# Optimization experiments

Measured on AMD Instinct MI355X. Metric: run time of the kernel, lower is better.

Reference implementation:

```python
import jax, jax.numpy as jnp
import numpy as np

N_NODES = 100000
N_EDGES = 1600000
N_GRAPHS = 1024
F_IN, H = 128, 32  # num_node_features, hidden_channels


def setup_inputs() -> dict:
    key = jax.random.key(0)
    ks = jax.random.split(key, 12)
    x = jax.random.normal(ks[0], (N_NODES, F_IN), dtype=jnp.float32)
    edge_index = jax.random.randint(ks[1], (2, N_EDGES), 0, N_NODES, dtype=jnp.int64)
    batch = jnp.sort(jax.random.randint(ks[2], (N_NODES,), 0, N_GRAPHS, dtype=jnp.int64))
    def lin(k, fi, fo):
        s = 1.0 / np.sqrt(fi)
        return jax.random.uniform(k, (fi, fo), jnp.float32, -s, s)
    return {
        "x": x, "edge_index": edge_index, "batch": batch,
        "W1": lin(ks[3], F_IN, H),      "b1": jnp.zeros((H,), jnp.float32),
        "W2": lin(ks[4], H, 2 * H),     "b2": jnp.zeros((2 * H,), jnp.float32),
        "W3": lin(ks[5], 2 * H, 4 * H), "b3": jnp.zeros((4 * H,), jnp.float32),
        "W_lin": lin(ks[6], 4 * H, 1),  "b_lin": jnp.zeros((1,), jnp.float32),
    }


def _gcn_conv(x, W, b, src, dst, dinv):
    # PyG GCNConv: x' = x @ W; add self-loops; sym-normalized scatter-add; + bias
    h = x @ W                                   # [N, Fo]
    coef = (dinv[src] * dinv[dst])[:, None]      # [E, 1]
    out = jax.ops.segment_sum(h[src] * coef, dst, num_segments=x.shape[0])
    out = out + h * (dinv * dinv)[:, None]       # self-loop contribution
    return out + b


def reference(x, edge_index, batch, W1, b1, W2, b2, W3, b3, W_lin, b_lin):
    src, dst = edge_index[0], edge_index[1]
    n = x.shape[0]
    # degree with self-loops (edge_weight = 1)
    deg = jax.ops.segment_sum(jnp.ones((src.shape[0],), x.dtype), dst, num_segments=n) + 1.0
    dinv = jax.lax.rsqrt(deg)
    h = jax.nn.relu(_gcn_conv(x, W1, b1, src, dst, dinv))
    h = jax.nn.relu(_gcn_conv(h, W2, b2, src, dst, dinv))
    h = _gcn_conv(h, W3, b3, src, dst, dinv)
    # global_mean_pool over graph ids
    sums = jax.ops.segment_sum(h, batch, num_segments=N_GRAPHS)
    cnts = jax.ops.segment_sum(jnp.ones((n,), h.dtype), batch, num_segments=N_GRAPHS)
    pooled = sums / jnp.maximum(cnts, 1.0)[:, None]
    # dropout skipped (inference / training=False)
    return pooled @ W_lin + b_lin
```

## Files before the change

### kernel.cpp

```cpp
#include <hip/hip_runtime.h>

static constexpr int F_IN = 128;
static constexpr int H1 = 32;
static constexpr int TPB = 256;
static constexpr int MAXBKT = 2048;

__global__ void bcount_kernel(const int* __restrict__ dst, int* __restrict__ bcnt,
                              int E, int nbkt) {
    __shared__ int h[MAXBKT];
    for (int t = threadIdx.x; t < nbkt; t += TPB) h[t] = 0;
    __syncthreads();
    const int CH = (E + gridDim.x - 1) / gridDim.x;
    const int lo = blockIdx.x * CH;
    const int hi = min(lo + CH, E);
    for (int i = lo + threadIdx.x; i < hi; i += TPB) atomicAdd(&h[dst[i] >> 6], 1);
    __syncthreads();
    for (int tt = threadIdx.x; tt < nbkt; tt += TPB) {
        int t = tt + blockIdx.x * 613;
        t -= (t >= nbkt) ? nbkt * (t / nbkt) : 0;
        if (h[t]) atomicAdd(&bcnt[t], h[t]);
    }
}

__global__ void bscan_kernel(const int* __restrict__ bcnt, int* __restrict__ bptr,
                             int* __restrict__ bcur, int nbkt, int E) {
    __shared__ int sh[512];
    __shared__ int carry;
    if (threadIdx.x == 0) carry = 0;
    __syncthreads();
    for (int base = 0; base < nbkt; base += 512) {
        int t = base + threadIdx.x;
        int v = (t < nbkt) ? bcnt[t] : 0;
        sh[threadIdx.x] = v;
        __syncthreads();
        for (int o = 1; o < 512; o <<= 1) {
            int u = (threadIdx.x >= o) ? sh[threadIdx.x - o] : 0;
            __syncthreads();
            sh[threadIdx.x] += u;
            __syncthreads();
        }
        if (t < nbkt) {
            int excl = carry + sh[threadIdx.x] - v;
            bptr[t] = excl;
            bcur[t] = excl;
        }
        __syncthreads();
        if (threadIdx.x == 0) carry += sh[511];
        __syncthreads();
    }
    if (threadIdx.x == 0) bptr[nbkt] = E;
}

__global__ void bfill_kernel(const int* __restrict__ src, const int* __restrict__ dst,
                             int* __restrict__ bcur, int* __restrict__ packed,
                             int E, int nbkt) {
    __shared__ int h[MAXBKT];
    for (int t = threadIdx.x; t < nbkt; t += TPB) h[t] = 0;
    __syncthreads();
    const int CH = (E + gridDim.x - 1) / gridDim.x;
    const int lo = blockIdx.x * CH;
    const int hi = min(lo + CH, E);
    for (int i = lo + threadIdx.x; i < hi; i += TPB) atomicAdd(&h[dst[i] >> 6], 1);
    __syncthreads();
    for (int tt = threadIdx.x; tt < nbkt; tt += TPB) {
        int t = tt + blockIdx.x * 613;
        t -= (t >= nbkt) ? nbkt * (t / nbkt) : 0;
        int c = h[t];
        h[t] = c ? atomicAdd(&bcur[t], c) : 0;
    }
    __syncthreads();
    for (int i = lo + threadIdx.x; i < hi; i += TPB) {
        int d = dst[i];
        int slot = atomicAdd(&h[d >> 6], 1);
        packed[slot] = (src[i] << 6) | (d & 63);
    }
}

__global__ void localize_kernel(const int* __restrict__ bptr, const int* __restrict__ packed,
                                int* __restrict__ csr_src, int* __restrict__ degi,
                                int* __restrict__ rowptr, float* __restrict__ dinv, int N) {
    __shared__ int lcnt[64];
    __shared__ int lcur[64];
    const int b = blockIdx.x;
    const int lo = bptr[b], hi = bptr[b + 1];
    if (threadIdx.x < 64) lcnt[threadIdx.x] = 0;
    __syncthreads();
    for (int i = lo + threadIdx.x; i < hi; i += TPB) atomicAdd(&lcnt[packed[i] & 63], 1);
    __syncthreads();
    if (threadIdx.x < 64) {
        int v = lcnt[threadIdx.x];
        int s = v;
#pragma unroll
        for (int o = 1; o < 64; o <<= 1) {
            int u = __shfl_up(s, o, 64);
            if ((threadIdx.x & 63) >= (unsigned)o) s += u;
        }
        int excl = s - v;
        lcur[threadIdx.x] = lo + excl;
        int node = b * 64 + threadIdx.x;
        if (node < N) {
            rowptr[node] = lo + excl;
            degi[node] = v;
            dinv[node] = 1.0f / sqrtf((float)v + 1.0f);
        }
    }
    __syncthreads();
    for (int i = lo + threadIdx.x; i < hi; i += TPB) {
        int e = packed[i];
        int slot = atomicAdd(&lcur[e & 63], 1);
        csr_src[slot] = e >> 6;
    }
}

__global__ void prep_kernel(const float* __restrict__ W3, const float* __restrict__ b3,
                            const float* __restrict__ Wl, const float* __restrict__ bl,
                            float* __restrict__ w3l) {
    int j = threadIdx.x;
    float acc = 0.0f;
#pragma unroll
    for (int k = 0; k < 128; ++k) acc = fmaf(W3[j * 128 + k], Wl[k], acc);
    w3l[j] = acc;
    if (j == 0) {
        float beta = bl[0];
        for (int f = 0; f < 128; ++f) beta = fmaf(b3[f], Wl[f], beta);
        w3l[64] = beta;
    }
}

__global__ void gemm1_kernel(const float* __restrict__ X, const float* __restrict__ W,
                             const float* __restrict__ dinv, float* __restrict__ T, int N) {
    __shared__ float S[4224];
    float* Ws = S;
    float (*Os)[36] = reinterpret_cast<float(*)[36]>(S);
    for (int t = threadIdx.x; t < F_IN * H1; t += TPB) Ws[t] = W[t];
    __syncthreads();
    const int c16 = threadIdx.x & 15;
    const int kh  = (threadIdx.x >> 4) & 1;
    const int g   = threadIdx.x >> 5;
    const int base = blockIdx.x * 64;
    const int r0 = base + g * 8;
    const int k4o = kh * 16;
    const float4* xr[8];
#pragma unroll
    for (int i = 0; i < 8; ++i) {
        int row = r0 + i;
        if (row >= N) row = N - 1;
        xr[i] = reinterpret_cast<const float4*>(X + (size_t)row * F_IN);
    }
    float acc0[8] = {0, 0, 0, 0, 0, 0, 0, 0};
    float acc1[8] = {0, 0, 0, 0, 0, 0, 0, 0};
#pragma unroll 4
    for (int k4 = 0; k4 < 16; ++k4) {
        const int kk = (k4 + k4o) * 4;
        float wa0 = Ws[(kk + 0) * H1 + c16];
        float wa1 = Ws[(kk + 1) * H1 + c16];
        float wa2 = Ws[(kk + 2) * H1 + c16];
        float wa3 = Ws[(kk + 3) * H1 + c16];
        float wb0 = Ws[(kk + 0) * H1 + c16 + 16];
        float wb1 = Ws[(kk + 1) * H1 + c16 + 16];
        float wb2 = Ws[(kk + 2) * H1 + c16 + 16];
        float wb3 = Ws[(kk + 3) * H1 + c16 + 16];
#pragma unroll
        for (int i = 0; i < 8; ++i) {
            float4 xv = xr[i][k4 + k4o];
            acc0[i] = fmaf(xv.x, wa0, acc0[i]);
            acc0[i] = fmaf(xv.y, wa1, acc0[i]);
            acc0[i] = fmaf(xv.z, wa2, acc0[i]);
            acc0[i] = fmaf(xv.w, wa3, acc0[i]);
            acc1[i] = fmaf(xv.x, wb0, acc1[i]);
            acc1[i] = fmaf(xv.y, wb1, acc1[i]);
            acc1[i] = fmaf(xv.z, wb2, acc1[i]);
            acc1[i] = fmaf(xv.w, wb3, acc1[i]);
        }
    }
#pragma unroll
    for (int i = 0; i < 8; ++i) {
        acc0[i] += __shfl_xor(acc0[i], 16);
        acc1[i] += __shfl_xor(acc1[i], 16);
    }
    __syncthreads();
    const int myc = c16 + kh * 16;
#pragma unroll
    for (int i = 0; i < 8; ++i) {
        int row = r0 + i;
        float dv = dinv[row < N ? row : (N - 1)];
        float v = kh ? acc1[i] : acc0[i];
        Os[g * 8 + i][myc] = v * dv;
    }
    __syncthreads();
#pragma unroll
    for (int it = 0; it < 2; ++it) {
        int flat = it * 256 + threadIdx.x;
        int f4 = (flat & 1) * 4;
        int row = (flat >> 1) & 63;
        int s = flat >> 7;
        int grow = base + row;
        if (grow < N) {
            float4 v = *reinterpret_cast<const float4*>(&Os[row][s * 8 + f4]);
            *reinterpret_cast<float4*>(&T[((size_t)s * N + grow) * 8 + f4]) = v;
        }
    }
}

template <bool HASBIAS>
__global__ void gather_s(const int* __restrict__ rowptr, const int* __restrict__ degi,
                         const int* __restrict__ csr, const float* __restrict__ dinv,
                         const float* __restrict__ b, const float* __restrict__ Tin,
                         float* __restrict__ Tout, int N) {
    const int cls = blockIdx.x & 3;
    const int b4 = blockIdx.x >> 2;
    const int nb4 = gridDim.x >> 2;
    const int f = threadIdx.x & 7;
    const int cl = threadIdx.x >> 3;
    const float* __restrict__ tab = Tin + (size_t)cls * N * 8;
    float* __restrict__ outp = Tout + (size_t)cls * N * 8;
    const float bias = HASBIAS ? b[cls * 8 + f] : 0.0f;
    for (int node = b4 * 32 + cl; node < N; node += nb4 * 32) {
        float dv = dinv[node];
        float acc = tab[(size_t)node * 8 + f];
        int j = rowptr[node];
        const int end = j + degi[node];
        for (; j + 8 <= end; j += 8) {
            int sidx = csr[j + f];
#pragma unroll
            for (int k = 0; k < 8; ++k) {
                int s = __shfl(sidx, k, 8);
                acc += tab[(size_t)s * 8 + f];
            }
        }
        if (j < end) {
            int myIdx = j + f;
            int sidx = (myIdx < end) ? csr[myIdx] : -1;
#pragma unroll
            for (int k = 0; k < 8; ++k) {
                int s = __shfl(sidx, k, 8);
                if (s >= 0) acc += tab[(size_t)s * 8 + f];
            }
        }
        float v;
        if (HASBIAS) v = fmaxf(fmaf(acc, dv, bias), 0.0f) * dv;
        else         v = acc * dv;
        outp[(size_t)node * 8 + f] = v;
    }
}

__global__ void gemm2z_kernel(const float* __restrict__ S1s, const float* __restrict__ W2,
                              const float* __restrict__ b2, const float* __restrict__ w3l,
                              const float* __restrict__ dinv, float* __restrict__ zp, int N) {
    __shared__ float W2s[H1 * 64];
    __shared__ float bw[64];
    __shared__ float wl[64];
    for (int t = threadIdx.x; t < H1 * 64; t += blockDim.x) W2s[t] = W2[t];
    if (threadIdx.x < 64) {
        bw[threadIdx.x] = b2[threadIdx.x];
        wl[threadIdx.x] = w3l[threadIdx.x];
    }
    __syncthreads();
    int node = blockIdx.x * (TPB / 32) + (threadIdx.x >> 5);
    int f = threadIdx.x & 31;
    if (node >= N) return;
    float s1 = S1s[((size_t)(f >> 3) * N + node) * 8 + (f & 7)];
    float d0 = bw[f], d1 = bw[f + 32];
#pragma unroll
    for (int k = 0; k < H1; ++k) {
        float sv = __shfl(s1, k, 32);
        d0 = fmaf(sv, W2s[k * 64 + f], d0);
        d1 = fmaf(sv, W2s[k * 64 + f + 32], d1);
    }
    float p = fmaxf(d0, 0.0f) * wl[f] + fmaxf(d1, 0.0f) * wl[f + 32];
#pragma unroll
    for (int o = 16; o > 0; o >>= 1) p += __shfl_down(p, o, 32);
    if (f == 0) zp[node] = p * dinv[node];
}

__global__ void gather_z_pool(const int* __restrict__ rowptr, const int* __restrict__ degi,
                              const int* __restrict__ csr_src, const float* __restrict__ dinv,
                              const float* __restrict__ zp, const int* __restrict__ batch,
                              float* __restrict__ sums, float* __restrict__ cnt, int N, int G) {
    __shared__ float accS[TPB];
    __shared__ float cntS[TPB];
    accS[threadIdx.x] = 0.0f;
    cntS[threadIdx.x] = 0.0f;
    __syncthreads();
    int i = blockIdx.x * TPB + threadIdx.x;
    int first = blockIdx.x * TPB;
    int b0 = batch[first < N ? first : (N - 1)];
    if (i < N) {
        float acc = zp[i];
        int j = rowptr[i];
        int end = j + degi[i];
        for (; j + 1 < end; j += 2) acc += zp[csr_src[j]] + zp[csr_src[j + 1]];
        if (j < end) acc += zp[csr_src[j]];
        float val = acc * dinv[i];
        int off = batch[i] - b0;
        if (off < TPB) {
            atomicAdd(&accS[off], val);
            atomicAdd(&cntS[off], 1.0f);
        } else {
            atomicAdd(&sums[batch[i]], val);
            atomicAdd(&cnt[batch[i]], 1.0f);
        }
    }
    __syncthreads();
    int g = b0 + threadIdx.x;
    if (g < G) {
        if (accS[threadIdx.x] != 0.0f) atomicAdd(&sums[g], accS[threadIdx.x]);
        if (cntS[threadIdx.x] != 0.0f) atomicAdd(&cnt[g], cntS[threadIdx.x]);
    }
}

__global__ void out_kernel(const float* __restrict__ sums, const float* __restrict__ cnt,
                           const float* __restrict__ w3l, float* __restrict__ out, int G) {
    int g = blockIdx.x * blockDim.x + threadIdx.x;
    if (g < G) out[g] = sums[g] / fmaxf(cnt[g], 1.0f) + w3l[64];
}

extern "C" void kernel_launch(void* const* d_in, const int* in_sizes, int n_in,
                              void* d_out, int out_size, void* d_ws, size_t ws_size,
                              hipStream_t stream) {
    const float* x     = (const float*)d_in[0];
    const int*   ei    = (const int*)d_in[1];
    const int*   batch = (const int*)d_in[2];
    const float* W1    = (const float*)d_in[3];
    const float* b1    = (const float*)d_in[4];
    const float* W2    = (const float*)d_in[5];
    const float* b2    = (const float*)d_in[6];
    const float* W3    = (const float*)d_in[7];
    const float* b3    = (const float*)d_in[8];
    const float* Wl    = (const float*)d_in[9];
    const float* bl    = (const float*)d_in[10];
    float* out = (float*)d_out;

    const int N = in_sizes[0] / F_IN;
    const int E = in_sizes[1] / 2;
    const int G = out_size;
    const int* src = ei;
    const int* dst = ei + E;
    const int nbkt = (N + 63) >> 6;

    int*   degi    = (int*)d_ws;
    int*   rowptr  = degi + N;
    int*   bcnt    = rowptr + N;
    int*   bptr    = bcnt + MAXBKT;
    int*   bcur    = bptr + MAXBKT;
    int*   packed  = bcur + MAXBKT;
    int*   csr_src = packed + E;
    float* dinv    = (float*)(csr_src + E);
    float* t1p     = dinv + N;
    float* g1p     = t1p + (size_t)N * H1;
    float* s1s     = g1p + (size_t)N * H1;
    float* zp      = s1s + (size_t)N * H1;
    float* w3l     = zp + N;
    float* sums    = w3l + 72;
    float* cnt     = sums + G;

    hipMemsetAsync(bcnt, 0, (size_t)MAXBKT * sizeof(int), stream);
    hipMemsetAsync(sums, 0, (size_t)2 * G * sizeof(float), stream);

    bcount_kernel<<<256, TPB, 0, stream>>>(dst, bcnt, E, nbkt);
    bscan_kernel<<<1, 512, 0, stream>>>(bcnt, bptr, bcur, nbkt, E);
    bfill_kernel<<<256, TPB, 0, stream>>>(src, dst, bcur, packed, E, nbkt);
    localize_kernel<<<nbkt, TPB, 0, stream>>>(bptr, packed, csr_src, degi, rowptr, dinv, N);

    prep_kernel<<<1, 64, 0, stream>>>(W3, b3, Wl, bl, w3l);

    gemm1_kernel<<<(N + 63) / 64, TPB, 0, stream>>>(x, W1, dinv, t1p, N);

    gather_s<true><<<4096, TPB, 0, stream>>>(rowptr, degi, csr_src, dinv, b1, t1p, g1p, N);

    gather_s<false><<<4096, TPB, 0, stream>>>(rowptr, degi, csr_src, dinv, nullptr, g1p, s1s, N);

    gemm2z_kernel<<<(N + 7) / 8, TPB, 0, stream>>>(s1s, W2, b2, w3l, dinv, zp, N);

    gather_z_pool<<<(N + TPB - 1) / TPB, TPB, 0, stream>>>(rowptr, degi, csr_src, dinv, zp,
                                                           batch, sums, cnt, N, G);
    out_kernel<<<(G + TPB - 1) / TPB, TPB, 0, stream>>>(sums, cnt, w3l, out, G);
}
```

Measured before the change: 244.4 us.

## Split bucket count/fill kernels into eight bucket classes per edge chunk

The bucket histogram and fill kernels now launch 2048 blocks. Each block covers one of 256 edge chunks and one of 8 bucket classes, so it keeps only a 256-entry shared histogram instead of one covering all buckets. This cuts the per-block shared-memory init and flush work, raises block count for occupancy, and makes writes to packed more localized per class. In exchange every edge's dst is read 8 times across blocks (src once), and the fill order within buckets changes.

```diff
diff --git a/kernel.cpp b/kernel.cpp
--- a/kernel.cpp
+++ b/kernel.cpp
@@ -5,20 +5,27 @@
 static constexpr int TPB = 256;
 static constexpr int MAXBKT = 2048;
 
-__global__ void bcount_kernel(const int* __restrict__ dst, int* __restrict__ bcnt,
-                              int E, int nbkt) {
-    __shared__ int h[MAXBKT];
-    for (int t = threadIdx.x; t < nbkt; t += TPB) h[t] = 0;
-    __syncthreads();
-    const int CH = (E + gridDim.x - 1) / gridDim.x;
-    const int lo = blockIdx.x * CH;
+__global__ void bcount_classed(const int* __restrict__ dst, int* __restrict__ bcnt,
+                               int E, int nbkt, int bpc) {
+    __shared__ int h[256];
+    const int r = blockIdx.x & 7;
+    const int chunk = blockIdx.x >> 3;
+    const int nch = gridDim.x >> 3;
+    const int CH = (E + nch - 1) / nch;
+    const int lo = chunk * CH;
     const int hi = min(lo + CH, E);
-    for (int i = lo + threadIdx.x; i < hi; i += TPB) atomicAdd(&h[dst[i] >> 6], 1);
-    __syncthreads();
-    for (int tt = threadIdx.x; tt < nbkt; tt += TPB) {
-        int t = tt + blockIdx.x * 613;
-        t -= (t >= nbkt) ? nbkt * (t / nbkt) : 0;
-        if (h[t]) atomicAdd(&bcnt[t], h[t]);
+    const int qbase = r * bpc;
+    if (threadIdx.x < bpc) h[threadIdx.x] = 0;
+    __syncthreads();
+    for (int i = lo + threadIdx.x; i < hi; i += TPB) {
+        unsigned q = (unsigned)((dst[i] >> 6) - qbase);
+        if (q < (unsigned)bpc) atomicAdd(&h[q], 1);
+    }
+    __syncthreads();
+    if (threadIdx.x < bpc) {
+        int c = h[threadIdx.x];
+        int b = qbase + threadIdx.x;
+        if (c && b < nbkt) atomicAdd(&bcnt[b], c);
     }
 }
 
@@ -51,28 +58,37 @@
     if (threadIdx.x == 0) bptr[nbkt] = E;
 }
 
-__global__ void bfill_kernel(const int* __restrict__ src, const int* __restrict__ dst,
-                             int* __restrict__ bcur, int* __restrict__ packed,
-                             int E, int nbkt) {
-    __shared__ int h[MAXBKT];
-    for (int t = threadIdx.x; t < nbkt; t += TPB) h[t] = 0;
-    __syncthreads();
-    const int CH = (E + gridDim.x - 1) / gridDim.x;
-    const int lo = blockIdx.x * CH;
+__global__ void bfill_classed(const int* __restrict__ src, const int* __restrict__ dst,
+                              int* __restrict__ bcur, int* __restrict__ packed,
+                              int E, int nbkt, int bpc) {
+    __shared__ int h[256];
+    const int r = blockIdx.x & 7;
+    const int chunk = blockIdx.x >> 3;
+    const int nch = gridDim.x >> 3;
+    const int CH = (E + nch - 1) / nch;
+    const int lo = chunk * CH;
     const int hi = min(lo + CH, E);
-    for (int i = lo + threadIdx.x; i < hi; i += TPB) atomicAdd(&h[dst[i] >> 6], 1);
-    __syncthreads();
-    for (int tt = threadIdx.x; tt < nbkt; tt += TPB) {
-        int t = tt + blockIdx.x * 613;
-        t -= (t >= nbkt) ? nbkt * (t / nbkt) : 0;
-        int c = h[t];
-        h[t] = c ? atomicAdd(&bcur[t], c) : 0;
+    const int qbase = r * bpc;
+    if (threadIdx.x < bpc) h[threadIdx.x] = 0;
+    __syncthreads();
+    for (int i = lo + threadIdx.x; i < hi; i += TPB) {
+        unsigned q = (unsigned)((dst[i] >> 6) - qbase);
+        if (q < (unsigned)bpc) atomicAdd(&h[q], 1);
+    }
+    __syncthreads();
+    if (threadIdx.x < bpc) {
+        int c = h[threadIdx.x];
+        int b = qbase + threadIdx.x;
+        h[threadIdx.x] = (c && b < nbkt) ? atomicAdd(&bcur[b], c) : 0;
     }
     __syncthreads();
     for (int i = lo + threadIdx.x; i < hi; i += TPB) {
         int d = dst[i];
-        int slot = atomicAdd(&h[d >> 6], 1);
-        packed[slot] = (src[i] << 6) | (d & 63);
+        unsigned q = (unsigned)((d >> 6) - qbase);
+        if (q < (unsigned)bpc) {
+            int slot = atomicAdd(&h[q], 1);
+            packed[slot] = (src[i] << 6) | (d & 63);
+        }
     }
 }
 
@@ -337,6 +353,7 @@
     const int* src = ei;
     const int* dst = ei + E;
     const int nbkt = (N + 63) >> 6;
+    const int bpc  = (nbkt + 7) >> 3;
 
     int*   degi    = (int*)d_ws;
     int*   rowptr  = degi + N;
@@ -357,9 +374,9 @@
     hipMemsetAsync(bcnt, 0, (size_t)MAXBKT * sizeof(int), stream);
     hipMemsetAsync(sums, 0, (size_t)2 * G * sizeof(float), stream);
 
-    bcount_kernel<<<256, TPB, 0, stream>>>(dst, bcnt, E, nbkt);
+    bcount_classed<<<2048, TPB, 0, stream>>>(dst, bcnt, E, nbkt, bpc);
     bscan_kernel<<<1, 512, 0, stream>>>(bcnt, bptr, bcur, nbkt, E);
-    bfill_kernel<<<256, TPB, 0, stream>>>(src, dst, bcur, packed, E, nbkt);
+    bfill_classed<<<2048, TPB, 0, stream>>>(src, dst, bcur, packed, E, nbkt, bpc);
     localize_kernel<<<nbkt, TPB, 0, stream>>>(bptr, packed, csr_src, degi, rowptr, dinv, N);
 
     prep_kernel<<<1, 64, 0, stream>>>(W3, b3, Wl, bl, w3l);
```

Result: slower. 260.8 us (+6.7%).
